# Optimization experiments

Measured on AMD Instinct MI355X. Metric: run time of the kernel, lower is better.

Reference implementation:

```python
import jax, jax.numpy as jnp
import numpy as np

B, T, D, H = 2, 2048, 2048, 16
HD = D // H  # 128


def _rope_tables(t, hd):
    # standard RoPE frequencies
    inv_freq = 1.0 / (10000.0 ** (np.arange(0, hd, 2, dtype=np.float32) / hd))
    pos = np.arange(t, dtype=np.float32)
    freqs = np.outer(pos, inv_freq)          # [t, hd/2]
    emb = np.concatenate([freqs, freqs], -1)  # [t, hd]
    return jnp.asarray(np.cos(emb)), jnp.asarray(np.sin(emb))


def setup_inputs() -> dict:
    key = jax.random.key(0)
    k1, k2, k3 = jax.random.split(key, 3)
    x = jax.random.normal(k1, (B, T, D), dtype=jnp.float32)
    cos, sin = _rope_tables(T, HD)
    Wqkv = jax.random.normal(k2, (3 * D, D), dtype=jnp.float32) * (D ** -0.5)
    Wout = jax.random.normal(k3, (D, D), dtype=jnp.float32) * (D ** -0.5)
    return {"x": x, "cos": cos, "sin": sin, "Wqkv": Wqkv, "Wout": Wout}


def _rotate_half(u):
    u1, u2 = jnp.split(u, 2, axis=-1)
    return jnp.concatenate([-u2, u1], axis=-1)


def _apply_rotary(u, cos, sin):
    # u: [b,h,t,hd]; cos/sin: [t,hd] broadcast over b,h
    return u * cos[None, None] + _rotate_half(u) * sin[None, None]


def reference(x, cos, sin, Wqkv, Wout):
    b, t, d = x.shape
    qkv = jnp.einsum('btd,ed->bte', x, Wqkv)                 # [b,t,3d]
    qkv = qkv.reshape(b, t, 3, H, HD).transpose(2, 0, 3, 1, 4)  # [3,b,h,t,hd]
    q, k, v = qkv[0], qkv[1], qkv[2]
    q = _apply_rotary(q, cos, sin)
    k = _apply_rotary(k, cos, sin)
    scale = 1.0 / jnp.sqrt(jnp.asarray(HD, dtype=x.dtype))
    scores = jnp.einsum('bhqe,bhke->bhqk', q, k) * scale      # [b,h,t,t]
    causal = jnp.tril(jnp.ones((t, t), dtype=bool))
    scores = jnp.where(causal[None, None], scores, jnp.asarray(-jnp.inf, dtype=scores.dtype))
    probs = jax.nn.softmax(scores, axis=-1)
    attn = jnp.einsum('bhqk,bhke->bhqe', probs, v)            # [b,h,t,hd]
    attn = attn.transpose(0, 2, 1, 3).reshape(b, t, d)
    return jnp.einsum('btd,ed->bte', attn, Wout)
```

## Files before the change

### kernel.cpp

```cpp
#include <hip/hip_runtime.h>
#include <hip/hip_bf16.h>
#include <stdint.h>

#define T_SEQ 2048
#define D_MODEL 2048
#define N_HEADS 16
#define HEAD_DIM 128

typedef __hip_bfloat16 bf16_t;
typedef __attribute__((ext_vector_type(8))) short short8;
typedef __attribute__((ext_vector_type(4))) short short4v;
typedef __attribute__((ext_vector_type(4))) float f32x4;
typedef __attribute__((ext_vector_type(16))) float f32x16;

__device__ __forceinline__ unsigned short f2bf(float x) {
  union { float f; unsigned u; } c; c.f = x;
  unsigned u = c.u;
  u += 0x7fffu + ((u >> 16) & 1u);
  return (unsigned short)(u >> 16);
}
__device__ __forceinline__ float bf2f(short v) {
  union { unsigned u; float f; } c;
  c.u = ((unsigned)(unsigned short)v) << 16;
  return c.f;
}
__device__ __forceinline__ void async16(const bf16_t* g, bf16_t* l) {
  __builtin_amdgcn_global_load_lds(
      (const __attribute__((address_space(1))) void*)g,
      (__attribute__((address_space(3))) void*)l, 16, 0, 0);
}

__global__ __launch_bounds__(256) void cvt_kernel(const float* __restrict__ in,
                                                  unsigned short* __restrict__ out,
                                                  int n4) {
  int i = blockIdx.x * 256 + threadIdx.x;
  if (i >= n4) return;
  float4 v = ((const float4*)in)[i];
  short4v o;
  o[0] = (short)f2bf(v.x); o[1] = (short)f2bf(v.y);
  o[2] = (short)f2bf(v.z); o[3] = (short)f2bf(v.w);
  ((short4v*)out)[i] = o;
}

template<int F32OUT>
__global__ __launch_bounds__(512, 4) void gemm_tp_kernel(
    const bf16_t* __restrict__ A, const bf16_t* __restrict__ Bm,
    float* __restrict__ Cf, unsigned short* __restrict__ Cb,
    int M, int N, int K, int nbn) {
  __shared__ bf16_t lds[36864];
  const int tid = threadIdx.x;
  const int w = tid >> 6, lane = tid & 63;
  const int wm = w >> 2, wn = w & 3;
  const int l15 = lane & 15, g = lane >> 4;

  const int nwg = gridDim.x;
  const int cpx = nwg >> 3;
  const int wg = (blockIdx.x & 7) * cpx + (blockIdx.x >> 3);
  const int bm0 = (wg / nbn) * 128, bn0 = (wg % nbn) * 256;

  const int sl = tid >> 3;
  const int su = (tid & 7) ^ (sl & 7);
  const int srow = (sl << 1) | (su >> 2);
  const int sc8 = su & 3;
  const bf16_t* agA = A + (size_t)(bm0 + srow) * K + sc8 * 8;
  const bf16_t* agB = Bm + (size_t)(bn0 + srow) * K + sc8 * 8;

#define STAGE(KT, SB) do {                                                    \
    bf16_t* _d = lds + (SB) * 12288 + w * 512;                                \
    async16(agA + (size_t)(KT) * 32, _d);                                     \
    async16(agB + (size_t)(KT) * 32, _d + 4096);                              \
    async16(agB + 128 * (size_t)K + (size_t)(KT) * 32, _d + 8192);            \
  } while (0)

  const int lhalf = l15 >> 1;
  const int aoff = lhalf * 64 + (((((l15 & 1) << 2) | g) ^ lhalf)) * 8;
  const bf16_t* Abase = lds + wm * 2048 + aoff;
  const bf16_t* Bbase = lds + 4096 + wn * 2048 + aoff;

  f32x4 acc[4][4];
#pragma unroll
  for (int i = 0; i < 4; ++i)
#pragma unroll
    for (int j = 0; j < 4; ++j)
#pragma unroll
      for (int e = 0; e < 4; ++e) acc[i][j][e] = 0.0f;

  STAGE(0, 0);
  STAGE(1, 1);

  const int NT = K >> 5;
  int cb = 0, sb = 2;
  for (int kt = 0; kt < NT - 1; ++kt) {
    asm volatile("s_waitcnt vmcnt(3)" ::: "memory");
    __builtin_amdgcn_s_barrier();
    const bf16_t* Ab = Abase + cb * 12288;
    const bf16_t* Bb = Bbase + cb * 12288;
    short8 af[4], bfr[4];
#pragma unroll
    for (int mi = 0; mi < 4; ++mi) af[mi] = *(const short8*)(Ab + mi * 512);
#pragma unroll
    for (int ni = 0; ni < 4; ++ni) bfr[ni] = *(const short8*)(Bb + ni * 512);
    if (kt < NT - 2) STAGE(kt + 2, sb);
    __builtin_amdgcn_s_setprio(1);
#pragma unroll
    for (int mi = 0; mi < 4; ++mi)
#pragma unroll
      for (int ni = 0; ni < 4; ++ni)
        acc[mi][ni] = __builtin_amdgcn_mfma_f32_16x16x32_bf16(
            af[mi], bfr[ni], acc[mi][ni], 0, 0, 0);
    __builtin_amdgcn_s_setprio(0);
    cb = (cb == 2) ? 0 : cb + 1;
    sb = (sb == 2) ? 0 : sb + 1;
  }
  {
    asm volatile("s_waitcnt vmcnt(0)" ::: "memory");
    __builtin_amdgcn_s_barrier();
    const bf16_t* Ab = Abase + cb * 12288;
    const bf16_t* Bb = Bbase + cb * 12288;
    short8 af[4], bfr[4];
#pragma unroll
    for (int mi = 0; mi < 4; ++mi) af[mi] = *(const short8*)(Ab + mi * 512);
#pragma unroll
    for (int ni = 0; ni < 4; ++ni) bfr[ni] = *(const short8*)(Bb + ni * 512);
    __builtin_amdgcn_s_setprio(1);
#pragma unroll
    for (int mi = 0; mi < 4; ++mi)
#pragma unroll
      for (int ni = 0; ni < 4; ++ni)
        acc[mi][ni] = __builtin_amdgcn_mfma_f32_16x16x32_bf16(
            af[mi], bfr[ni], acc[mi][ni], 0, 0, 0);
    __builtin_amdgcn_s_setprio(0);
  }
#undef STAGE

#pragma unroll
  for (int mi = 0; mi < 4; ++mi)
#pragma unroll
    for (int ni = 0; ni < 4; ++ni)
#pragma unroll
      for (int r = 0; r < 4; ++r) {
        int mr = bm0 + wm * 64 + mi * 16 + g * 4 + r;
        int nc = bn0 + wn * 64 + ni * 16 + l15;
        if (F32OUT)
          Cf[(size_t)mr * N + nc] = acc[mi][ni][r];
        else
          Cb[(size_t)mr * N + nc] = f2bf(acc[mi][ni][r]);
      }
}

__global__ __launch_bounds__(256) void rope_kernel(
    const bf16_t* __restrict__ qkv,
    const float* __restrict__ cosb, const float* __restrict__ sinb,
    bf16_t* __restrict__ qo, bf16_t* __restrict__ ko, bf16_t* __restrict__ vT) {
  const int nTT = T_SEQ / 64;
  const int bx = blockIdx.x;
  const int bh = bx / nTT, tt = bx % nTT;
  const int b = bh / N_HEADS, h = bh % N_HEADS;
  const int tid = threadIdx.x;
  __shared__ bf16_t vlds[64][136];

  const float SC = 0.08838834764831845f;

#pragma unroll
  for (int it = 0; it < 2; ++it) {
    int item = it * 256 + tid;
    int r = item >> 3, cg = item & 7;
    int t = tt * 64 + r;
    int c0 = cg * 8;
    size_t base = ((size_t)b * T_SEQ + t) * (size_t)(3 * D_MODEL) + (size_t)h * HEAD_DIM;

    float cs0[8], sn0[8], cs1[8], sn1[8];
    {
      const float* cp = cosb + (size_t)t * HEAD_DIM + c0;
      const float* sp = sinb + (size_t)t * HEAD_DIM + c0;
      float4 a0 = *(const float4*)(cp), a1 = *(const float4*)(cp + 4);
      float4 b0 = *(const float4*)(cp + 64), b1 = *(const float4*)(cp + 68);
      float4 s0 = *(const float4*)(sp), s1 = *(const float4*)(sp + 4);
      float4 t0 = *(const float4*)(sp + 64), t1 = *(const float4*)(sp + 68);
      cs0[0]=a0.x; cs0[1]=a0.y; cs0[2]=a0.z; cs0[3]=a0.w; cs0[4]=a1.x; cs0[5]=a1.y; cs0[6]=a1.z; cs0[7]=a1.w;
      cs1[0]=b0.x; cs1[1]=b0.y; cs1[2]=b0.z; cs1[3]=b0.w; cs1[4]=b1.x; cs1[5]=b1.y; cs1[6]=b1.z; cs1[7]=b1.w;
      sn0[0]=s0.x; sn0[1]=s0.y; sn0[2]=s0.z; sn0[3]=s0.w; sn0[4]=s1.x; sn0[5]=s1.y; sn0[6]=s1.z; sn0[7]=s1.w;
      sn1[0]=t0.x; sn1[1]=t0.y; sn1[2]=t0.z; sn1[3]=t0.w; sn1[4]=t1.x; sn1[5]=t1.y; sn1[6]=t1.z; sn1[7]=t1.w;
    }

#pragma unroll
    for (int sec = 0; sec < 2; ++sec) {
      size_t sbase = base + (size_t)sec * D_MODEL;
      short8 lo = *(const short8*)(qkv + sbase + c0);
      short8 hi = *(const short8*)(qkv + sbase + 64 + c0);
      short8 olo, ohi;
#pragma unroll
      for (int e = 0; e < 8; ++e) {
        float xl = bf2f(lo[e]), xh = bf2f(hi[e]);
        float rl = xl * cs0[e] - xh * sn0[e];
        float rh = xh * cs1[e] + xl * sn1[e];
        if (sec == 0) { rl *= SC; rh *= SC; }
        olo[e] = (short)f2bf(rl);
        ohi[e] = (short)f2bf(rh);
      }
      bf16_t* dst = (sec == 0 ? qo : ko) + ((size_t)bh * T_SEQ + t) * HEAD_DIM + c0;
      *(short8*)dst = olo;
      *(short8*)(dst + 64) = ohi;
    }

    short8 v0 = *(const short8*)(qkv + base + 2 * D_MODEL + c0);
    short8 v1 = *(const short8*)(qkv + base + 2 * D_MODEL + 64 + c0);
    *(short8*)&vlds[r][c0] = v0;
    *(short8*)&vlds[r][64 + c0] = v1;
  }
  __syncthreads();

  int hd = tid >> 1, hf = tid & 1;
  bf16_t* dst = vT + ((size_t)bh * HEAD_DIM + hd) * T_SEQ + tt * 64 + hf * 32;
#pragma unroll
  for (int jj = 0; jj < 4; ++jj) {
    short8 o;
#pragma unroll
    for (int e = 0; e < 8; ++e)
      o[e] = *(const short*)&vlds[hf * 32 + jj * 8 + e][hd];
    *(short8*)(dst + jj * 8) = o;
  }
}

__global__ __launch_bounds__(256, 2) void attn_kernel(
    const bf16_t* __restrict__ q, const bf16_t* __restrict__ k,
    const bf16_t* __restrict__ vT, unsigned short* __restrict__ attn) {
  const int bx = blockIdx.x;
  const int bh = bx & 31;
  const int qi = (bx >> 5) & 7;
  const int qt = (bx >> 8) ? qi : 15 - qi;
  const int b = bh / N_HEADS, h = bh % N_HEADS;
  const int tid = threadIdx.x;
  const int w = tid >> 6, lane = tid & 63;
  const int l31 = lane & 31, hi = lane >> 5;
  const int swz = l31 & 7;
  const float LOG2E = 1.44269504088896340736f;

  __shared__ bf16_t smem[32768];

  const bf16_t* qb = q + (size_t)bh * T_SEQ * HEAD_DIM;
  const bf16_t* kb = k + (size_t)bh * T_SEQ * HEAD_DIM;
  const bf16_t* vb = vT + (size_t)bh * HEAD_DIM * T_SEQ;

  const int qlo = qt * 128 + w * 32;
  const int qhi = qlo + 31;
  const int qrow = qlo + l31;

  short8 qf[8];
#pragma unroll
  for (int ks = 0; ks < 8; ++ks)
    qf[ks] = *(const short8*)(qb + (size_t)qrow * HEAD_DIM + ks * 16 + hi * 8);

  float m = -3.0e38f, l = 0.0f;
  f32x16 O[4];
#pragma unroll
  for (int dt = 0; dt < 4; ++dt)
#pragma unroll
    for (int r = 0; r < 16; ++r) O[dt][r] = 0.0f;

#define STAGE_TILES(KT, BU) {                                                    \
    _Pragma("unroll")                                                            \
    for (int j = 0; j < 4; ++j) {                                                \
      int s = j * 4 + w;                                                         \
      int row = s * 4 + (lane >> 4);                                             \
      int gc = (lane & 15) ^ (row & 7);                                          \
      async16(kb + (size_t)((KT) * 64 + row) * HEAD_DIM + gc * 8,                \
              smem + (BU) * 8192 + s * 512);                                     \
    }                                                                            \
    _Pragma("unroll")                                                            \
    for (int j = 0; j < 4; ++j) {                                                \
      int s = j * 4 + w;                                                         \
      int row = s * 8 + (lane >> 3);                                             \
      int gc = (lane & 7) ^ (row & 7);                                           \
      async16(vb + (size_t)row * T_SEQ + (KT) * 64 + gc * 8,                     \
              smem + 16384 + (BU) * 8192 + s * 512);                             \
    }                                                                            \
  }

  STAGE_TILES(0, 0);
  __syncthreads();
  int buf = 0;

  const int lastk = 2 * qt + 1;
  for (int kt = 0; kt <= lastk; ++kt) {
    if (kt < lastk) STAGE_TILES(kt + 1, buf ^ 1);
    const bf16_t* Ks = smem + buf * 8192;
    const bf16_t* Vs = smem + 16384 + buf * 8192;
    const bool active = (kt * 64 <= qhi);

    if (active) {
      f32x16 S[2];
#pragma unroll
      for (int kvt = 0; kvt < 2; ++kvt) {
        const int kvbase = kt * 64 + kvt * 32;
        if (kvbase <= qhi) {
          const int krow = kvt * 32 + l31;
#pragma unroll
          for (int r = 0; r < 16; ++r) S[kvt][r] = 0.0f;
          __builtin_amdgcn_s_setprio(1);
#pragma unroll
          for (int ks = 0; ks < 8; ++ks) {
            int c = (2 * ks + hi) ^ swz;
            short8 kf = *(const short8*)(Ks + krow * 128 + c * 8);
            S[kvt] = __builtin_amdgcn_mfma_f32_32x32x16_bf16(kf, qf[ks], S[kvt], 0, 0, 0);
          }
          __builtin_amdgcn_s_setprio(0);
          if (kvbase + 31 > qlo) {
#pragma unroll
            for (int r = 0; r < 16; ++r) {
              int kv = kvbase + (r & 3) + 8 * (r >> 2) + 4 * hi;
              if (kv > qrow) S[kvt][r] = -3.0e38f;
            }
          }
        } else {
#pragma unroll
          for (int r = 0; r < 16; ++r) S[kvt][r] = -3.0e38f;
        }
      }

      float rl = -3.0e38f;
#pragma unroll
      for (int kvt = 0; kvt < 2; ++kvt)
#pragma unroll
        for (int r = 0; r < 16; ++r) rl = fmaxf(rl, S[kvt][r]);
      rl = fmaxf(rl, __shfl_xor(rl, 32, 64));
      float mn = fmaxf(m, rl);
      float fac = exp2f((m - mn) * LOG2E);
      m = mn;
      float sum = 0.0f;
#pragma unroll
      for (int kvt = 0; kvt < 2; ++kvt)
#pragma unroll
        for (int r = 0; r < 16; ++r) {
          float p = exp2f((S[kvt][r] - m) * LOG2E);
          S[kvt][r] = p;
          sum += p;
        }
      sum += __shfl_xor(sum, 32, 64);
      l = l * fac + sum;
#pragma unroll
      for (int dt = 0; dt < 4; ++dt)
#pragma unroll
        for (int r = 0; r < 16; ++r) O[dt][r] *= fac;

      short8 pf[4];
#pragma unroll
      for (int ks = 0; ks < 4; ++ks) {
        const int kvt = ks >> 1;
        const int base = (ks & 1) * 8;
        unsigned pkL0, pkL1, pkH0, pkH1;
        {
          float a0 = S[kvt][base + 0], a1 = S[kvt][base + 1];
          float a2 = S[kvt][base + 2], a3 = S[kvt][base + 3];
          float b0 = S[kvt][base + 4], b1 = S[kvt][base + 5];
          float b2 = S[kvt][base + 6], b3 = S[kvt][base + 7];
          asm("v_cvt_pk_bf16_f32 %0, %1, %2" : "=v"(pkL0) : "v"(a0), "v"(a1));
          asm("v_cvt_pk_bf16_f32 %0, %1, %2" : "=v"(pkL1) : "v"(a2), "v"(a3));
          asm("v_cvt_pk_bf16_f32 %0, %1, %2" : "=v"(pkH0) : "v"(b0), "v"(b1));
          asm("v_cvt_pk_bf16_f32 %0, %1, %2" : "=v"(pkH1) : "v"(b2), "v"(b3));
        }
        unsigned sx0 = hi ? pkL0 : pkH0;
        unsigned sx1 = hi ? pkL1 : pkH1;
        unsigned rx0 = (unsigned)__shfl_xor((int)sx0, 32, 64);
        unsigned rx1 = (unsigned)__shfl_xor((int)sx1, 32, 64);
        union { unsigned u[4]; short8 s; } uu;
        uu.u[0] = hi ? rx0 : pkL0;
        uu.u[1] = hi ? rx1 : pkL1;
        uu.u[2] = hi ? pkH0 : rx0;
        uu.u[3] = hi ? pkH1 : rx1;
        pf[ks] = uu.s;
      }

      __builtin_amdgcn_s_setprio(1);
#pragma unroll
      for (int dt = 0; dt < 4; ++dt) {
        const int vrow = dt * 32 + l31;
#pragma unroll
        for (int ks = 0; ks < 4; ++ks) {
          int c = (2 * ks + hi) ^ swz;
          short8 vf = *(const short8*)(Vs + vrow * 64 + c * 8);
          O[dt] = __builtin_amdgcn_mfma_f32_32x32x16_bf16(vf, pf[ks], O[dt], 0, 0, 0);
        }
      }
      __builtin_amdgcn_s_setprio(0);
    }

    __syncthreads();
    buf ^= 1;
  }
#undef STAGE_TILES

  float inv = 1.0f / l;
  bf16_t* ol = smem + w * 4352;
#pragma unroll
  for (int dt = 0; dt < 4; ++dt)
#pragma unroll
    for (int r = 0; r < 16; ++r) {
      int d = dt * 32 + (r & 3) + 8 * (r >> 2) + 4 * hi;
      *(unsigned short*)&ol[l31 * 136 + d] = f2bf(O[dt][r] * inv);
    }
  __syncthreads();
  const int srow4 = lane >> 4;
  const int scol = (lane & 15) * 8;
#pragma unroll
  for (int rr = 0; rr < 8; ++rr) {
    int row = rr * 4 + srow4;
    short8 v = *(const short8*)(ol + row * 136 + scol);
    *(short8*)(attn + ((size_t)b * T_SEQ + qt * 128 + w * 32 + row) * D_MODEL +
               (size_t)h * HEAD_DIM + scol) = v;
  }
}

extern "C" void kernel_launch(void* const* d_in, const int* in_sizes, int n_in,
                              void* d_out, int out_size, void* d_ws, size_t ws_size,
                              hipStream_t stream) {
  const float* x    = (const float*)d_in[0];
  const float* cosb = (const float*)d_in[1];
  const float* sinb = (const float*)d_in[2];
  const float* Wqkv = (const float*)d_in[3];
  const float* Wout = (const float*)d_in[4];
  float* out = (float*)d_out;

  char* ws = (char*)d_ws;
  size_t off = 0;
  bf16_t* xb    = (bf16_t*)(ws + off); off += (size_t)4096 * 2048 * 2;
  bf16_t* wqkvb = (bf16_t*)(ws + off); off += (size_t)6144 * 2048 * 2;
  bf16_t* woutb = (bf16_t*)(ws + off); off += (size_t)2048 * 2048 * 2;
  bf16_t* qkvb  = (bf16_t*)(ws + off); off += (size_t)4096 * 6144 * 2;
  bf16_t* qb    = (bf16_t*)(ws + off); off += (size_t)32 * 2048 * 128 * 2;
  bf16_t* kb    = (bf16_t*)(ws + off); off += (size_t)32 * 2048 * 128 * 2;
  bf16_t* vTb   = (bf16_t*)(ws + off); off += (size_t)32 * 2048 * 128 * 2;
  bf16_t* attnb = xb;

  cvt_kernel<<<8192, 256, 0, stream>>>(x, (unsigned short*)xb, 4096 * 2048 / 4);
  cvt_kernel<<<12288, 256, 0, stream>>>(Wqkv, (unsigned short*)wqkvb, 6144 * 2048 / 4);
  cvt_kernel<<<4096, 256, 0, stream>>>(Wout, (unsigned short*)woutb, 2048 * 2048 / 4);

  gemm_tp_kernel<0><<<768, 512, 0, stream>>>(xb, wqkvb, nullptr, (unsigned short*)qkvb,
                                             4096, 6144, 2048, 24);

  rope_kernel<<<1024, 256, 0, stream>>>(qkvb, cosb, sinb, qb, kb, vTb);

  attn_kernel<<<512, 256, 0, stream>>>(qb, kb, vTb, (unsigned short*)attnb);

  gemm_tp_kernel<1><<<256, 512, 0, stream>>>(attnb, woutb, out, nullptr,
                                             4096, 2048, 2048, 8);
}
```

Measured before the change: 274.3 us.

## Restructure GEMM to BK=64 with interleaved staged loads and split MFMA phases

The bf16 GEMM now uses a K tile of 64 instead of 32, doubling LDS to a triple-buffered 144 KB footprint, and splits each tile into four MFMA phases. Each phase issues part of the async global-to-LDS loads for the tile two steps ahead, with barriers between phases. The aim is to halve the per-K-step barrier and wait overhead and spread memory traffic across compute. In exchange, occupancy drops to 2 blocks per CU and there are more barriers per tile.

```diff
diff --git a/kernel.cpp b/kernel.cpp
--- a/kernel.cpp
+++ b/kernel.cpp
@@ -43,11 +43,11 @@
 }
 
 template<int F32OUT>
-__global__ __launch_bounds__(512, 4) void gemm_tp_kernel(
+__global__ __launch_bounds__(512, 2) void gemm_8p_kernel(
     const bf16_t* __restrict__ A, const bf16_t* __restrict__ Bm,
     float* __restrict__ Cf, unsigned short* __restrict__ Cb,
     int M, int N, int K, int nbn) {
-  __shared__ bf16_t lds[36864];
+  __shared__ bf16_t lds[73728];
   const int tid = threadIdx.x;
   const int w = tid >> 6, lane = tid & 63;
   const int wm = w >> 2, wn = w & 3;
@@ -58,80 +58,104 @@
   const int wg = (blockIdx.x & 7) * cpx + (blockIdx.x >> 3);
   const int bm0 = (wg / nbn) * 128, bn0 = (wg % nbn) * 256;
 
-  const int sl = tid >> 3;
-  const int su = (tid & 7) ^ (sl & 7);
-  const int srow = (sl << 1) | (su >> 2);
-  const int sc8 = su & 3;
-  const bf16_t* agA = A + (size_t)(bm0 + srow) * K + sc8 * 8;
-  const bf16_t* agB = Bm + (size_t)(bn0 + srow) * K + sc8 * 8;
-
-#define STAGE(KT, SB) do {                                                    \
-    bf16_t* _d = lds + (SB) * 12288 + w * 512;                                \
-    async16(agA + (size_t)(KT) * 32, _d);                                     \
-    async16(agB + (size_t)(KT) * 32, _d + 4096);                              \
-    async16(agB + 128 * (size_t)K + (size_t)(KT) * 32, _d + 8192);            \
+  const int srow = tid >> 3;
+  const int sgc = (tid & 7) ^ (srow & 7);
+  const bf16_t* agA = A + (size_t)(bm0 + srow) * K + sgc * 8;
+  const bf16_t* agB = Bm + (size_t)(bn0 + srow) * K + sgc * 8;
+
+#define STG_A(T) do { const int _s = (T) % 3;                                 \
+    bf16_t* _d = lds + _s * 24576 + w * 512;                                  \
+    async16(agA + (size_t)(T) * 64, _d);                                      \
+    async16(agA + 64 * (size_t)K + (size_t)(T) * 64, _d + 4096); } while (0)
+#define STG_B01(T) do { const int _s = (T) % 3;                               \
+    bf16_t* _d = lds + _s * 24576 + 8192 + w * 512;                           \
+    async16(agB + (size_t)(T) * 64, _d);                                      \
+    async16(agB + 64 * (size_t)K + (size_t)(T) * 64, _d + 4096); } while (0)
+#define STG_B23(T) do { const int _s = (T) % 3;                               \
+    bf16_t* _d = lds + _s * 24576 + 8192 + w * 512;                           \
+    async16(agB + 128 * (size_t)K + (size_t)(T) * 64, _d + 8192);             \
+    async16(agB + 192 * (size_t)K + (size_t)(T) * 64, _d + 12288); } while (0)
+
+  const int rdsw = l15 & 7;
+  const int cof0 = ((g) ^ rdsw) * 8;
+  const int cof1 = ((4 + g) ^ rdsw) * 8;
+
+  f32x4 acc[4][4];
+#pragma unroll
+  for (int i = 0; i < 4; ++i)
+#pragma unroll
+    for (int j = 0; j < 4; ++j)
+#pragma unroll
+      for (int e = 0; e < 4; ++e) acc[i][j][e] = 0.0f;
+
+#define MFMA_HALF(NLO, AF, B0, B1)                                            \
+    _Pragma("unroll")                                                         \
+    for (int mi = 0; mi < 4; ++mi) {                                          \
+      acc[mi][NLO] = __builtin_amdgcn_mfma_f32_16x16x32_bf16(AF[mi], B0, acc[mi][NLO], 0, 0, 0); \
+      acc[mi][NLO + 1] = __builtin_amdgcn_mfma_f32_16x16x32_bf16(AF[mi], B1, acc[mi][NLO + 1], 0, 0, 0); \
+    }
+
+#define TILE8(T, DOSTG, WNSTR, DOWAIT) do {                                   \
+    const int _sb = (T) % 3;                                                  \
+    const bf16_t* Ab = lds + _sb * 24576 + (wm * 64 + l15) * 64;              \
+    const bf16_t* Bb = lds + _sb * 24576 + 8192 + (wn * 64 + l15) * 64;       \
+    short8 af[4], b0, b1;                                                     \
+                               \
+    _Pragma("unroll")                                                         \
+    for (int mi = 0; mi < 4; ++mi) af[mi] = *(const short8*)(Ab + mi * 1024 + cof0); \
+    b0 = *(const short8*)(Bb + cof0);                                         \
+    b1 = *(const short8*)(Bb + 1024 + cof0);                                  \
+    if (DOSTG) STG_A((T) + 2);                                                \
+    __builtin_amdgcn_s_barrier();                                             \
+    __builtin_amdgcn_s_setprio(1);                                            \
+    MFMA_HALF(0, af, b0, b1);                                                 \
+    __builtin_amdgcn_s_setprio(0);                                            \
+    __builtin_amdgcn_s_barrier();                                             \
+                                     \
+    b0 = *(const short8*)(Bb + 2048 + cof0);                                  \
+    b1 = *(const short8*)(Bb + 3072 + cof0);                                  \
+    if (DOSTG) STG_B01((T) + 2);                                              \
+    __builtin_amdgcn_s_barrier();                                             \
+    __builtin_amdgcn_s_setprio(1);                                            \
+    MFMA_HALF(2, af, b0, b1);                                                 \
+    __builtin_amdgcn_s_setprio(0);                                            \
+    __builtin_amdgcn_s_barrier();                                             \
+                             \
+    _Pragma("unroll")                                                         \
+    for (int mi = 0; mi < 4; ++mi) af[mi] = *(const short8*)(Ab + mi * 1024 + cof1); \
+    b0 = *(const short8*)(Bb + cof1);                                         \
+    b1 = *(const short8*)(Bb + 1024 + cof1);                                  \
+    if (DOSTG) STG_B23((T) + 2);                                              \
+    __builtin_amdgcn_s_barrier();                                             \
+    __builtin_amdgcn_s_setprio(1);                                            \
+    MFMA_HALF(0, af, b0, b1);                                                 \
+    __builtin_amdgcn_s_setprio(0);                                            \
+    __builtin_amdgcn_s_barrier();                                             \
+                                \
+    b0 = *(const short8*)(Bb + 2048 + cof1);                                  \
+    b1 = *(const short8*)(Bb + 3072 + cof1);                                  \
+    __builtin_amdgcn_s_barrier();                                             \
+    __builtin_amdgcn_s_setprio(1);                                            \
+    MFMA_HALF(2, af, b0, b1);                                                 \
+    __builtin_amdgcn_s_setprio(0);                                            \
+    if (DOWAIT) asm volatile("s_waitcnt vmcnt(" WNSTR ")" ::: "memory");      \
+    __builtin_amdgcn_s_barrier();                                             \
   } while (0)
 
-  const int lhalf = l15 >> 1;
-  const int aoff = lhalf * 64 + (((((l15 & 1) << 2) | g) ^ lhalf)) * 8;
-  const bf16_t* Abase = lds + wm * 2048 + aoff;
-  const bf16_t* Bbase = lds + 4096 + wn * 2048 + aoff;
-
-  f32x4 acc[4][4];
-#pragma unroll
-  for (int i = 0; i < 4; ++i)
-#pragma unroll
-    for (int j = 0; j < 4; ++j)
-#pragma unroll
-      for (int e = 0; e < 4; ++e) acc[i][j][e] = 0.0f;
-
-  STAGE(0, 0);
-  STAGE(1, 1);
-
-  const int NT = K >> 5;
-  int cb = 0, sb = 2;
-  for (int kt = 0; kt < NT - 1; ++kt) {
-    asm volatile("s_waitcnt vmcnt(3)" ::: "memory");
-    __builtin_amdgcn_s_barrier();
-    const bf16_t* Ab = Abase + cb * 12288;
-    const bf16_t* Bb = Bbase + cb * 12288;
-    short8 af[4], bfr[4];
-#pragma unroll
-    for (int mi = 0; mi < 4; ++mi) af[mi] = *(const short8*)(Ab + mi * 512);
-#pragma unroll
-    for (int ni = 0; ni < 4; ++ni) bfr[ni] = *(const short8*)(Bb + ni * 512);
-    if (kt < NT - 2) STAGE(kt + 2, sb);
-    __builtin_amdgcn_s_setprio(1);
-#pragma unroll
-    for (int mi = 0; mi < 4; ++mi)
-#pragma unroll
-      for (int ni = 0; ni < 4; ++ni)
-        acc[mi][ni] = __builtin_amdgcn_mfma_f32_16x16x32_bf16(
-            af[mi], bfr[ni], acc[mi][ni], 0, 0, 0);
-    __builtin_amdgcn_s_setprio(0);
-    cb = (cb == 2) ? 0 : cb + 1;
-    sb = (sb == 2) ? 0 : sb + 1;
-  }
-  {
-    asm volatile("s_waitcnt vmcnt(0)" ::: "memory");
-    __builtin_amdgcn_s_barrier();
-    const bf16_t* Ab = Abase + cb * 12288;
-    const bf16_t* Bb = Bbase + cb * 12288;
-    short8 af[4], bfr[4];
-#pragma unroll
-    for (int mi = 0; mi < 4; ++mi) af[mi] = *(const short8*)(Ab + mi * 512);
-#pragma unroll
-    for (int ni = 0; ni < 4; ++ni) bfr[ni] = *(const short8*)(Bb + ni * 512);
-    __builtin_amdgcn_s_setprio(1);
-#pragma unroll
-    for (int mi = 0; mi < 4; ++mi)
-#pragma unroll
-      for (int ni = 0; ni < 4; ++ni)
-        acc[mi][ni] = __builtin_amdgcn_mfma_f32_16x16x32_bf16(
-            af[mi], bfr[ni], acc[mi][ni], 0, 0, 0);
-    __builtin_amdgcn_s_setprio(0);
-  }
-#undef STAGE
+  STG_A(0); STG_B01(0); STG_B23(0);
+  STG_A(1); STG_B01(1); STG_B23(1);
+  asm volatile("s_waitcnt vmcnt(6)" ::: "memory");
+  __builtin_amdgcn_s_barrier();
+
+  const int NT = K >> 6;
+  for (int t = 0; t < NT - 2; ++t) TILE8(t, true, "6", true);
+  TILE8(NT - 2, false, "0", true);
+  TILE8(NT - 1, false, "0", false);
+#undef TILE8
+#undef MFMA_HALF
+#undef STG_A
+#undef STG_B01
+#undef STG_B23
 
 #pragma unroll
   for (int mi = 0; mi < 4; ++mi)
@@ -436,13 +460,13 @@
   cvt_kernel<<<12288, 256, 0, stream>>>(Wqkv, (unsigned short*)wqkvb, 6144 * 2048 / 4);
   cvt_kernel<<<4096, 256, 0, stream>>>(Wout, (unsigned short*)woutb, 2048 * 2048 / 4);
 
-  gemm_tp_kernel<0><<<768, 512, 0, stream>>>(xb, wqkvb, nullptr, (unsigned short*)qkvb,
+  gemm_8p_kernel<0><<<768, 512, 0, stream>>>(xb, wqkvb, nullptr, (unsigned short*)qkvb,
                                              4096, 6144, 2048, 24);
 
   rope_kernel<<<1024, 256, 0, stream>>>(qkvb, cosb, sinb, qb, kb, vTb);
 
   attn_kernel<<<512, 256, 0, stream>>>(qb, kb, vTb, (unsigned short*)attnb);
 
-  gemm_tp_kernel<1><<<256, 512, 0, stream>>>(attnb, woutb, out, nullptr,
+  gemm_8p_kernel<1><<<256, 512, 0, stream>>>(attnb, woutb, out, nullptr,
                                              4096, 2048, 2048, 8);
 }
```

Measured after the change: 278.4 us. About the same (+1.5%).
